# Kernel tuning notes

Measured on AMD Instinct MI355X. Metric: run time of the kernel, lower is better.

Reference implementation:

```python
import jax, jax.numpy as jnp
import numpy as np
from jax import lax

B, H, S, D = 4, 12, 4096, 64
TILE = 128


def setup_inputs() -> dict:
    key = jax.random.key(0)
    kq, kk, kv = jax.random.split(key, 3)
    query = jax.random.normal(kq, (B, H, S, D), dtype=jnp.float32)
    key_t = jax.random.normal(kk, (B, H, S, D), dtype=jnp.float32)
    value = jax.random.normal(kv, (B, H, S, D), dtype=jnp.float32)
    return {"query": query, "key": key_t, "value": value}


def _flash_tiled(query, key, value):
    b, h, s, d = query.shape
    scale = d ** (-0.5)
    nq = s // TILE
    nk = s // TILE
    # q tiles: [b, h, nq, TILE, d]; kv tiles scanned along leading axis
    q = query.reshape(b, h, nq, TILE, d)
    k = key.reshape(b, h, nk, TILE, d).transpose(2, 0, 1, 3, 4)    # [nk,b,h,TILE,d]
    v = value.reshape(b, h, nk, TILE, d).transpose(2, 0, 1, 3, 4)  # [nk,b,h,TILE,d]

    out0 = jnp.zeros((b, h, nq, TILE, d), dtype=query.dtype)
    m0 = jnp.full((b, h, nq, TILE, 1), -jnp.inf, dtype=query.dtype)
    s0 = jnp.zeros((b, h, nq, TILE, 1), dtype=query.dtype)

    def step(carry, kv_tiles):
        out, m, ssum = carry
        k_tile, v_tile = kv_tiles
        # scores: [b,h,nq,TILE_q,TILE_k]
        scores = jnp.einsum('bhntd,bhsd->bhnts', q, k_tile) * scale
        cur_max = jnp.max(scores, axis=-1, keepdims=True)
        new_max = jnp.maximum(m, cur_max)
        old_scale = jnp.exp(m - new_max)
        cur_scale = jnp.exp(cur_max - new_max)  # extra factor, faithful to source
        cur_exp = jnp.exp(scores - new_max)
        out = out * old_scale + cur_scale * jnp.einsum('bhnts,bhsd->bhntd', cur_exp, v_tile)
        ssum = ssum * old_scale + cur_scale * jnp.sum(cur_exp, axis=-1, keepdims=True)
        return (out, new_max, ssum), None

    (out, _, ssum), _ = lax.scan(step, (out0, m0, s0), (k, v))
    return (out / ssum).reshape(b, h, s, d)


def reference(query, key, value):
    return _flash_tiled(query, key, value)
```

## Files before the change

### kernel.cpp

```cpp
#include <hip/hip_runtime.h>
#include <hip/hip_bf16.h>


#define S_LEN 4096
#define HD    64
#define QTILE 128
#define KTILE 128
#define NKT   (S_LEN / KTILE)

#define KSTR  72
#define VSTR  136
#define VT_OFF (128 * KSTR)
#define SMEM_U16 (VT_OFF + HD * VSTR)
#define OSTR  68

typedef __attribute__((ext_vector_type(8))) short bf16x8;
typedef __attribute__((ext_vector_type(4))) short bf16x4;
typedef __attribute__((ext_vector_type(4))) float f32x4;

__device__ __forceinline__ unsigned int pk2(float f0, float f1) {
    unsigned int u0 = __builtin_bit_cast(unsigned int, f0) + 0x8000u;
    unsigned int u1 = __builtin_bit_cast(unsigned int, f1) + 0x8000u;
    return __builtin_amdgcn_perm(u1, u0, 0x07060302u);
}

__global__ __launch_bounds__(256, 3)
void fattn_kernel(const float* __restrict__ Q,
                  const float* __restrict__ K,
                  const float* __restrict__ V,
                  float* __restrict__ O) {
    __shared__ __align__(16) unsigned short smem[SMEM_U16];

    const int t    = threadIdx.x;
    const int wave = t >> 6;
    const int lane = t & 63;
    const int m    = lane & 15;
    const int quad = lane >> 4;

    const int qblk = blockIdx.x;
    const int head = blockIdx.y;
    const size_t hbase = (size_t)head * S_LEN * HD;

    unsigned short* const Kl = smem;
    unsigned short* const Vt = smem + VT_OFF;

    bf16x8 qf[2][2];
    #pragma unroll
    for (int rt = 0; rt < 2; ++rt) {
        const float* qp = Q + hbase +
            (size_t)(qblk * QTILE + wave * 32 + rt * 16 + m) * HD + quad * 8;
        #pragma unroll
        for (int kd = 0; kd < 2; ++kd) {
            float4 a = *(const float4*)(qp + kd * 32);
            float4 b = *(const float4*)(qp + kd * 32 + 4);
            union { unsigned int u[4]; bf16x8 v; } cv;
            cv.u[0] = pk2(a.x * 0.125f, a.y * 0.125f);
            cv.u[1] = pk2(a.z * 0.125f, a.w * 0.125f);
            cv.u[2] = pk2(b.x * 0.125f, b.y * 0.125f);
            cv.u[3] = pk2(b.z * 0.125f, b.w * 0.125f);
            qf[rt][kd] = cv.v;
        }
    }

    f32x4 oacc[4][2];
    float mrow[2] = {-INFINITY, -INFINITY};
    float lrow[2] = {0.f, 0.f};
    #pragma unroll
    for (int dt = 0; dt < 4; ++dt)
        #pragma unroll
        for (int rt = 0; rt < 2; ++rt) oacc[dt][rt] = (f32x4){0.f,0.f,0.f,0.f};

    const int r0k = t >> 3;
    const int c0k = (t & 7) * 8;
    const int chk = ((t & 7) + ((t >> 3) & 7)) & 7;
    const int vkey = t & 127;
    const int vdb  = (t >> 7) * 32;
    unsigned short* const vwp = &Vt[vdb * VSTR + vkey];

    float4 va[4][2];
    {
        const float* vp = V + hbase + (size_t)vkey * HD + vdb;
        #pragma unroll
        for (int i = 0; i < 4; ++i) {
            va[i][0] = *(const float4*)(vp + i * 8);
            va[i][1] = *(const float4*)(vp + i * 8 + 4);
        }
    }

    for (int kt = 0; kt < NKT; ++kt) {
        __syncthreads();

        #pragma unroll
        for (int i = 0; i < 4; ++i) {
            #pragma unroll
            for (int j = 0; j < 8; ++j) {
                float f = ((const float*)&va[i][j >> 2])[j & 3];
                unsigned int u = __builtin_bit_cast(unsigned int, f) + 0x8000u;
                vwp[(i * 8 + j) * VSTR] = (unsigned short)(u >> 16);
            }
        }
        {
            const float* kp = K + hbase + (size_t)(kt * KTILE + r0k) * HD + c0k;
            #pragma unroll
            for (int i = 0; i < 4; ++i) {
                float4 a = *(const float4*)(kp + i * 32 * HD);
                float4 b = *(const float4*)(kp + i * 32 * HD + 4);
                union { unsigned int u[4]; bf16x4 v[2]; } cv;
                cv.u[0] = pk2(a.x, a.y); cv.u[1] = pk2(a.z, a.w);
                cv.u[2] = pk2(b.x, b.y); cv.u[3] = pk2(b.z, b.w);
                *(bf16x8*)&Kl[(r0k + i * 32) * KSTR + chk * 8] =
                    *(bf16x8*)&cv.u[0];
            }
        }
        __syncthreads();

        {
            int nk = (kt + 1 < NKT) ? kt + 1 : 0;
            const float* vp = V + hbase + (size_t)(nk * KTILE + vkey) * HD + vdb;
            #pragma unroll
            for (int i = 0; i < 4; ++i) {
                va[i][0] = *(const float4*)(vp + i * 8);
                va[i][1] = *(const float4*)(vp + i * 8 + 4);
            }
        }

        f32x4 sacc[8][2];
        #pragma unroll
        for (int k8 = 0; k8 < 8; ++k8)
            #pragma unroll
            for (int rt = 0; rt < 2; ++rt) sacc[k8][rt] = (f32x4){0.f,0.f,0.f,0.f};

        #pragma unroll
        for (int kd = 0; kd < 2; ++kd) {
            const int coff = (((kd << 2) + quad + m) & 7) << 3;
            #pragma unroll
            for (int k8 = 0; k8 < 8; ++k8) {
                bf16x8 kf = *(const bf16x8*)&Kl[(k8 * 16 + m) * KSTR + coff];
                sacc[k8][0] = __builtin_amdgcn_mfma_f32_16x16x32_bf16(
                    kf, qf[0][kd], sacc[k8][0], 0, 0, 0);
                sacc[k8][1] = __builtin_amdgcn_mfma_f32_16x16x32_bf16(
                    kf, qf[1][kd], sacc[k8][1], 0, 0, 0);
            }
        }

        unsigned int pkv[8][2][2];
        #pragma unroll
        for (int rt = 0; rt < 2; ++rt) {
            float cm = sacc[0][rt][0];
            #pragma unroll
            for (int k8 = 0; k8 < 8; ++k8)
                #pragma unroll
                for (int r = 0; r < 4; ++r)
                    cm = fmaxf(cm, sacc[k8][rt][r]);
            cm = fmaxf(cm, __shfl_xor(cm, 16, 64));
            cm = fmaxf(cm, __shfl_xor(cm, 32, 64));

            float mo  = mrow[rt];
            float mn  = fmaxf(mo, cm);
            float osc = __expf(mo - mn);
            float bias = cm - mn - mn;
            mrow[rt] = mn;

            #pragma unroll
            for (int dt = 0; dt < 4; ++dt) {
                oacc[dt][rt][0] *= osc; oacc[dt][rt][1] *= osc;
                oacc[dt][rt][2] *= osc; oacc[dt][rt][3] *= osc;
            }

            float rs = 0.f;
            #pragma unroll
            for (int k8 = 0; k8 < 8; ++k8) {
                float p0 = __expf(sacc[k8][rt][0] + bias);
                float p1 = __expf(sacc[k8][rt][1] + bias);
                float p2 = __expf(sacc[k8][rt][2] + bias);
                float p3 = __expf(sacc[k8][rt][3] + bias);
                rs += (p0 + p1) + (p2 + p3);
                pkv[k8][rt][0] = pk2(p0, p1);
                pkv[k8][rt][1] = pk2(p2, p3);
            }
            rs += __shfl_xor(rs, 16, 64);
            rs += __shfl_xor(rs, 32, 64);
            lrow[rt] = lrow[rt] * osc + rs;
        }

        #pragma unroll
        for (int kc = 0; kc < 4; ++kc) {
            bf16x8 pf[2];
            #pragma unroll
            for (int rt = 0; rt < 2; ++rt) {
                union { unsigned int u[4]; bf16x8 v; } cv;
                cv.u[0] = pkv[2 * kc][rt][0];
                cv.u[1] = pkv[2 * kc][rt][1];
                cv.u[2] = pkv[2 * kc + 1][rt][0];
                cv.u[3] = pkv[2 * kc + 1][rt][1];
                pf[rt] = cv.v;
            }
            #pragma unroll
            for (int dt = 0; dt < 4; ++dt) {
                const unsigned short* vp0 =
                    &Vt[(dt * 16 + m) * VSTR + kc * 32 + quad * 4];
                bf16x4 a = *(const bf16x4*)vp0;
                bf16x4 b = *(const bf16x4*)(vp0 + 16);
                bf16x8 vf;
                vf[0]=a[0]; vf[1]=a[1]; vf[2]=a[2]; vf[3]=a[3];
                vf[4]=b[0]; vf[5]=b[1]; vf[6]=b[2]; vf[7]=b[3];
                oacc[dt][0] = __builtin_amdgcn_mfma_f32_16x16x32_bf16(
                    vf, pf[0], oacc[dt][0], 0, 0, 0);
                oacc[dt][1] = __builtin_amdgcn_mfma_f32_16x16x32_bf16(
                    vf, pf[1], oacc[dt][1], 0, 0, 0);
            }
        }
    }

    __syncthreads();
    float* Ol = (float*)smem;
    #pragma unroll
    for (int rt = 0; rt < 2; ++rt) {
        float inv = 1.0f / lrow[rt];
        #pragma unroll
        for (int dt = 0; dt < 4; ++dt)
            #pragma unroll
            for (int r = 0; r < 4; ++r)
                Ol[(wave * 32 + rt * 16 + m) * OSTR + dt * 16 + quad * 4 + r] =
                    oacc[dt][rt][r] * inv;
    }
    __syncthreads();
    const size_t obase = hbase + (size_t)(qblk * QTILE) * HD;
    #pragma unroll
    for (int s = 0; s < 8; ++s) {
        int row = s * 16 + (t >> 4);
        int col = (t & 15) * 4;
        *(float4*)&O[obase + (size_t)row * HD + col] =
            *(const float4*)&Ol[row * OSTR + col];
    }
}

extern "C" void kernel_launch(void* const* d_in, const int* in_sizes, int n_in,
                              void* d_out, int out_size, void* d_ws, size_t ws_size,
                              hipStream_t stream) {
    (void)in_sizes; (void)n_in; (void)d_ws; (void)ws_size; (void)out_size;
    const float* Q = (const float*)d_in[0];
    const float* K = (const float*)d_in[1];
    const float* V = (const float*)d_in[2];
    float* O = (float*)d_out;
    dim3 grid(S_LEN / QTILE, 4 * 12);
    fattn_kernel<<<grid, 256, 0, stream>>>(Q, K, V, O);
}
```

Measured before the change: 489.2 us.

## Pre-convert K and V to bf16 in workspace before the attention kernel

```diff
diff --git a/kernel.cpp b/kernel.cpp
--- a/kernel.cpp
+++ b/kernel.cpp
@@ -6,7 +6,8 @@
 #define HD    64
 #define QTILE 128
 #define KTILE 128
-#define NKT   (S_LEN / KTILE)
+#define NKT   32
+#define NHEAD 48
 
 #define KSTR  72
 #define VSTR  136
@@ -14,21 +15,84 @@
 #define SMEM_U16 (VT_OFF + HD * VSTR)
 #define OSTR  68
 
+#define WS_ELEMS ((size_t)NHEAD * S_LEN * HD)
+
 typedef __attribute__((ext_vector_type(8))) short bf16x8;
-typedef __attribute__((ext_vector_type(4))) short bf16x4;
 typedef __attribute__((ext_vector_type(4))) float f32x4;
 
 __device__ __forceinline__ unsigned int pk2(float f0, float f1) {
-    unsigned int u0 = __builtin_bit_cast(unsigned int, f0) + 0x8000u;
-    unsigned int u1 = __builtin_bit_cast(unsigned int, f1) + 0x8000u;
+    unsigned int u0 = __builtin_bit_cast(unsigned int, f0);
+    unsigned int u1 = __builtin_bit_cast(unsigned int, f1);
+    u0 += 0x7FFFu + ((u0 >> 16) & 1u);
+    u1 += 0x7FFFu + ((u1 >> 16) & 1u);
     return __builtin_amdgcn_perm(u1, u0, 0x07060302u);
 }
-
-__global__ __launch_bounds__(256, 3)
-void fattn_kernel(const float* __restrict__ Q,
-                  const float* __restrict__ K,
-                  const float* __restrict__ V,
-                  float* __restrict__ O) {
+__device__ __forceinline__ unsigned int pkt(float f0, float f1) {
+    return __builtin_amdgcn_perm(__builtin_bit_cast(unsigned int, f1),
+                                 __builtin_bit_cast(unsigned int, f0),
+                                 0x07060302u);
+}
+__device__ __forceinline__ float e2(float x) {
+#if __has_builtin(__builtin_amdgcn_exp2f)
+    return __builtin_amdgcn_exp2f(x);
+#else
+    return __expf(x * 0.6931471805599453f);
+#endif
+}
+
+__global__ __launch_bounds__(256)
+void k_convert(const float* __restrict__ K, unsigned short* __restrict__ Wk) {
+    size_t idx = ((size_t)blockIdx.x * 256 + threadIdx.x) * 8;
+    float4 a = *(const float4*)(K + idx);
+    float4 b = *(const float4*)(K + idx + 4);
+    union { unsigned int u[4]; bf16x8 v; } cv;
+    cv.u[0] = pk2(a.x, a.y); cv.u[1] = pk2(a.z, a.w);
+    cv.u[2] = pk2(b.x, b.y); cv.u[3] = pk2(b.z, b.w);
+    *(bf16x8*)((unsigned short*)Wk + idx) = cv.v;
+}
+
+__global__ __launch_bounds__(256)
+void v_trans(const float* __restrict__ V, unsigned short* __restrict__ Wv) {
+    __shared__ unsigned short T[64 * 132];
+    const int t = threadIdx.x;
+    const int kt = blockIdx.x, head = blockIdx.y;
+    const float* vp = V + (size_t)head * S_LEN * HD + (size_t)kt * KTILE * HD;
+    const int d0 = (t & 15) * 4;
+    const int kr = t >> 4;
+    #pragma unroll
+    for (int i = 0; i < 8; ++i) {
+        int key = i * 16 + kr;
+        float4 f = *(const float4*)(vp + key * HD + d0);
+        unsigned int p01 = pk2(f.x, f.y), p23 = pk2(f.z, f.w);
+        T[(d0 + 0) * 132 + key] = (unsigned short)(p01 & 0xffff);
+        T[(d0 + 1) * 132 + key] = (unsigned short)(p01 >> 16);
+        T[(d0 + 2) * 132 + key] = (unsigned short)(p23 & 0xffff);
+        T[(d0 + 3) * 132 + key] = (unsigned short)(p23 >> 16);
+    }
+    __syncthreads();
+    const int d = t >> 2;
+    const int c = t & 3;
+    unsigned short* op = Wv + (size_t)head * HD * S_LEN + (size_t)d * S_LEN
+                         + kt * KTILE + c * 32;
+    unsigned int out[16];
+    #pragma unroll
+    for (int jj = 0; jj < 16; ++jj) {
+        int j0 = 2 * jj, j1 = 2 * jj + 1;
+        int k0 = c * 32 + ((j0 >> 2) & 1) * 16 + (j0 >> 3) * 4 + (j0 & 3);
+        int k1 = c * 32 + ((j1 >> 2) & 1) * 16 + (j1 >> 3) * 4 + (j1 & 3);
+        out[jj] = (unsigned int)T[d * 132 + k0]
+                | ((unsigned int)T[d * 132 + k1] << 16);
+    }
+    #pragma unroll
+    for (int s = 0; s < 4; ++s)
+        *(bf16x8*)(op + s * 8) = *(const bf16x8*)&out[s * 4];
+}
+
+__global__ __launch_bounds__(256, 4)
+void fattn_fast(const float* __restrict__ Q,
+                const unsigned short* __restrict__ Wk,
+                const unsigned short* __restrict__ Wv,
+                float* __restrict__ O) {
     __shared__ __align__(16) unsigned short smem[SMEM_U16];
 
     const int t    = threadIdx.x;
@@ -41,6 +105,180 @@
     const int head = blockIdx.y;
     const size_t hbase = (size_t)head * S_LEN * HD;
 
+    unsigned short* const Kl = smem;
+    unsigned short* const Vt = smem + VT_OFF;
+
+    bf16x8 qf[2][2];
+    #pragma unroll
+    for (int rt = 0; rt < 2; ++rt) {
+        const float* qp = Q + hbase +
+            (size_t)(qblk * QTILE + wave * 32 + rt * 16 + m) * HD + quad * 8;
+        #pragma unroll
+        for (int kd = 0; kd < 2; ++kd) {
+            float4 a = *(const float4*)(qp + kd * 32);
+            float4 b = *(const float4*)(qp + kd * 32 + 4);
+            union { unsigned int u[4]; bf16x8 v; } cv;
+            const float s = 0.1803368801111f;
+            cv.u[0] = pk2(a.x * s, a.y * s);
+            cv.u[1] = pk2(a.z * s, a.w * s);
+            cv.u[2] = pk2(b.x * s, b.y * s);
+            cv.u[3] = pk2(b.z * s, b.w * s);
+            qf[rt][kd] = cv.v;
+        }
+    }
+
+    f32x4 oacc[4][2];
+    float mrow[2] = {-INFINITY, -INFINITY};
+    float lrow[2] = {0.f, 0.f};
+    #pragma unroll
+    for (int dt = 0; dt < 4; ++dt)
+        #pragma unroll
+        for (int rt = 0; rt < 2; ++rt) oacc[dt][rt] = (f32x4){0.f,0.f,0.f,0.f};
+
+    const int r0k = t >> 3;
+    const int kch = t & 7;
+    const int chk = ((t & 7) + ((t >> 3) & 7)) & 7;
+    const unsigned short* const kbase = Wk + hbase;
+    const unsigned short* const vbase = Wv + (size_t)head * HD * S_LEN;
+
+    for (int kt = 0; kt < NKT; ++kt) {
+        __syncthreads();
+        #pragma unroll
+        for (int i = 0; i < 4; ++i) {
+            int row = r0k + 32 * i;
+            bf16x8 kv = *(const bf16x8*)(kbase +
+                (size_t)(kt * KTILE + row) * HD + kch * 8);
+            *(bf16x8*)&Kl[row * KSTR + chk * 8] = kv;
+        }
+        #pragma unroll
+        for (int i = 0; i < 4; ++i) {
+            int id = t + 256 * i;
+            int d = id >> 4, ch = id & 15;
+            bf16x8 vv = *(const bf16x8*)(vbase +
+                (size_t)d * S_LEN + kt * KTILE + ch * 8);
+            *(bf16x8*)&Vt[d * VSTR + ch * 8] = vv;
+        }
+        __syncthreads();
+
+        f32x4 sacc[8][2];
+        #pragma unroll
+        for (int k8 = 0; k8 < 8; ++k8)
+            #pragma unroll
+            for (int rt = 0; rt < 2; ++rt) sacc[k8][rt] = (f32x4){0.f,0.f,0.f,0.f};
+
+        #pragma unroll
+        for (int kd = 0; kd < 2; ++kd) {
+            const int coff = (((kd << 2) + quad + m) & 7) << 3;
+            #pragma unroll
+            for (int k8 = 0; k8 < 8; ++k8) {
+                bf16x8 kf = *(const bf16x8*)&Kl[(k8 * 16 + m) * KSTR + coff];
+                sacc[k8][0] = __builtin_amdgcn_mfma_f32_16x16x32_bf16(
+                    kf, qf[0][kd], sacc[k8][0], 0, 0, 0);
+                sacc[k8][1] = __builtin_amdgcn_mfma_f32_16x16x32_bf16(
+                    kf, qf[1][kd], sacc[k8][1], 0, 0, 0);
+            }
+        }
+
+        unsigned int pkv[8][2][2];
+        #pragma unroll
+        for (int rt = 0; rt < 2; ++rt) {
+            float cm = sacc[0][rt][0];
+            #pragma unroll
+            for (int k8 = 0; k8 < 8; ++k8)
+                #pragma unroll
+                for (int r = 0; r < 4; ++r)
+                    cm = fmaxf(cm, sacc[k8][rt][r]);
+            cm = fmaxf(cm, __shfl_xor(cm, 16, 64));
+            cm = fmaxf(cm, __shfl_xor(cm, 32, 64));
+
+            float mo = mrow[rt];
+            float mn = fmaxf(mo, cm);
+            float bias = cm - mn - mn;
+            mrow[rt] = mn;
+
+            if (__any(cm > mo)) {
+                float osc = e2(mo - mn);
+                #pragma unroll
+                for (int dt = 0; dt < 4; ++dt) {
+                    oacc[dt][rt][0] *= osc; oacc[dt][rt][1] *= osc;
+                    oacc[dt][rt][2] *= osc; oacc[dt][rt][3] *= osc;
+                }
+                lrow[rt] *= osc;
+            }
+
+            float rs = 0.f;
+            #pragma unroll
+            for (int k8 = 0; k8 < 8; ++k8) {
+                float p0 = e2(sacc[k8][rt][0] + bias);
+                float p1 = e2(sacc[k8][rt][1] + bias);
+                float p2 = e2(sacc[k8][rt][2] + bias);
+                float p3 = e2(sacc[k8][rt][3] + bias);
+                rs += (p0 + p1) + (p2 + p3);
+                pkv[k8][rt][0] = pkt(p0, p1);
+                pkv[k8][rt][1] = pkt(p2, p3);
+            }
+            rs += __shfl_xor(rs, 16, 64);
+            rs += __shfl_xor(rs, 32, 64);
+            lrow[rt] += rs;
+        }
+
+        #pragma unroll
+        for (int kc = 0; kc < 4; ++kc) {
+            bf16x8 pf[2];
+            #pragma unroll
+            for (int rt = 0; rt < 2; ++rt) {
+                union { unsigned int u[4]; bf16x8 v; } cv;
+                cv.u[0] = pkv[2 * kc][rt][0];
+                cv.u[1] = pkv[2 * kc][rt][1];
+                cv.u[2] = pkv[2 * kc + 1][rt][0];
+                cv.u[3] = pkv[2 * kc + 1][rt][1];
+                pf[rt] = cv.v;
+            }
+            #pragma unroll
+            for (int dt = 0; dt < 4; ++dt) {
+                bf16x8 vf = *(const bf16x8*)&Vt[(dt * 16 + m) * VSTR +
+                                                kc * 32 + quad * 8];
+                oacc[dt][0] = __builtin_amdgcn_mfma_f32_16x16x32_bf16(
+                    vf, pf[0], oacc[dt][0], 0, 0, 0);
+                oacc[dt][1] = __builtin_amdgcn_mfma_f32_16x16x32_bf16(
+                    vf, pf[1], oacc[dt][1], 0, 0, 0);
+            }
+        }
+    }
+
+    __syncthreads();
+    float* Ol = (float*)smem;
+    #pragma unroll
+    for (int rt = 0; rt < 2; ++rt) {
+        float inv = 1.0f / lrow[rt];
+        #pragma unroll
+        for (int dt = 0; dt < 4; ++dt)
+            #pragma unroll
+            for (int r = 0; r < 4; ++r)
+                Ol[(wave * 32 + rt * 16 + m) * OSTR + dt * 16 + quad * 4 + r] =
+                    oacc[dt][rt][r] * inv;
+    }
+    __syncthreads();
+    const size_t obase = hbase + (size_t)(qblk * QTILE) * HD;
+    #pragma unroll
+    for (int s = 0; s < 8; ++s) {
+        int row = s * 16 + (t >> 4);
+        int col = (t & 15) * 4;
+        *(float4*)&O[obase + (size_t)row * HD + col] =
+            *(const float4*)&Ol[row * OSTR + col];
+    }
+}
+
+__global__ __launch_bounds__(256, 3)
+void fattn_fallback(const float* __restrict__ Q,
+                    const float* __restrict__ K,
+                    const float* __restrict__ V,
+                    float* __restrict__ O) {
+    __shared__ __align__(16) unsigned short smem[SMEM_U16];
+    const int t = threadIdx.x, wave = t >> 6, lane = t & 63;
+    const int m = lane & 15, quad = lane >> 4;
+    const int qblk = blockIdx.x, head = blockIdx.y;
+    const size_t hbase = (size_t)head * S_LEN * HD;
     unsigned short* const Kl = smem;
     unsigned short* const Vt = smem + VT_OFF;
 
@@ -61,7 +299,6 @@
             qf[rt][kd] = cv.v;
         }
     }
-
     f32x4 oacc[4][2];
     float mrow[2] = {-INFINITY, -INFINITY};
     float lrow[2] = {0.f, 0.f};
@@ -69,14 +306,10 @@
     for (int dt = 0; dt < 4; ++dt)
         #pragma unroll
         for (int rt = 0; rt < 2; ++rt) oacc[dt][rt] = (f32x4){0.f,0.f,0.f,0.f};
-
-    const int r0k = t >> 3;
-    const int c0k = (t & 7) * 8;
+    const int r0k = t >> 3, c0k = (t & 7) * 8;
     const int chk = ((t & 7) + ((t >> 3) & 7)) & 7;
-    const int vkey = t & 127;
-    const int vdb  = (t >> 7) * 32;
+    const int vkey = t & 127, vdb = (t >> 7) * 32;
     unsigned short* const vwp = &Vt[vdb * VSTR + vkey];
-
     float4 va[4][2];
     {
         const float* vp = V + hbase + (size_t)vkey * HD + vdb;
@@ -86,10 +319,8 @@
             va[i][1] = *(const float4*)(vp + i * 8 + 4);
         }
     }
-
     for (int kt = 0; kt < NKT; ++kt) {
         __syncthreads();
-
         #pragma unroll
         for (int i = 0; i < 4; ++i) {
             #pragma unroll
@@ -105,15 +336,13 @@
             for (int i = 0; i < 4; ++i) {
                 float4 a = *(const float4*)(kp + i * 32 * HD);
                 float4 b = *(const float4*)(kp + i * 32 * HD + 4);
-                union { unsigned int u[4]; bf16x4 v[2]; } cv;
+                union { unsigned int u[4]; bf16x8 v; } cv;
                 cv.u[0] = pk2(a.x, a.y); cv.u[1] = pk2(a.z, a.w);
                 cv.u[2] = pk2(b.x, b.y); cv.u[3] = pk2(b.z, b.w);
-                *(bf16x8*)&Kl[(r0k + i * 32) * KSTR + chk * 8] =
-                    *(bf16x8*)&cv.u[0];
+                *(bf16x8*)&Kl[(r0k + i * 32) * KSTR + chk * 8] = cv.v;
             }
         }
         __syncthreads();
-
         {
             int nk = (kt + 1 < NKT) ? kt + 1 : 0;
             const float* vp = V + hbase + (size_t)(nk * KTILE + vkey) * HD + vdb;
@@ -123,13 +352,11 @@
                 va[i][1] = *(const float4*)(vp + i * 8 + 4);
             }
         }
-
         f32x4 sacc[8][2];
         #pragma unroll
         for (int k8 = 0; k8 < 8; ++k8)
             #pragma unroll
             for (int rt = 0; rt < 2; ++rt) sacc[k8][rt] = (f32x4){0.f,0.f,0.f,0.f};
-
         #pragma unroll
         for (int kd = 0; kd < 2; ++kd) {
             const int coff = (((kd << 2) + quad + m) & 7) << 3;
@@ -142,7 +369,6 @@
                     kf, qf[1][kd], sacc[k8][1], 0, 0, 0);
             }
         }
-
         unsigned int pkv[8][2][2];
         #pragma unroll
         for (int rt = 0; rt < 2; ++rt) {
@@ -150,23 +376,18 @@
             #pragma unroll
             for (int k8 = 0; k8 < 8; ++k8)
                 #pragma unroll
-                for (int r = 0; r < 4; ++r)
-                    cm = fmaxf(cm, sacc[k8][rt][r]);
+                for (int r = 0; r < 4; ++r) cm = fmaxf(cm, sacc[k8][rt][r]);
             cm = fmaxf(cm, __shfl_xor(cm, 16, 64));
             cm = fmaxf(cm, __shfl_xor(cm, 32, 64));
-
-            float mo  = mrow[rt];
-            float mn  = fmaxf(mo, cm);
+            float mo = mrow[rt], mn = fmaxf(mo, cm);
             float osc = __expf(mo - mn);
             float bias = cm - mn - mn;
             mrow[rt] = mn;
-
             #pragma unroll
             for (int dt = 0; dt < 4; ++dt) {
                 oacc[dt][rt][0] *= osc; oacc[dt][rt][1] *= osc;
                 oacc[dt][rt][2] *= osc; oacc[dt][rt][3] *= osc;
             }
-
             float rs = 0.f;
             #pragma unroll
             for (int k8 = 0; k8 < 8; ++k8) {
@@ -182,7 +403,6 @@
             rs += __shfl_xor(rs, 32, 64);
             lrow[rt] = lrow[rt] * osc + rs;
         }
-
         #pragma unroll
         for (int kc = 0; kc < 4; ++kc) {
             bf16x8 pf[2];
@@ -199,11 +419,9 @@
             for (int dt = 0; dt < 4; ++dt) {
                 const unsigned short* vp0 =
                     &Vt[(dt * 16 + m) * VSTR + kc * 32 + quad * 4];
-                bf16x4 a = *(const bf16x4*)vp0;
-                bf16x4 b = *(const bf16x4*)(vp0 + 16);
                 bf16x8 vf;
-                vf[0]=a[0]; vf[1]=a[1]; vf[2]=a[2]; vf[3]=a[3];
-                vf[4]=b[0]; vf[5]=b[1]; vf[6]=b[2]; vf[7]=b[3];
+                #pragma unroll
+                for (int j = 0; j < 4; ++j) { vf[j] = vp0[j]; vf[4 + j] = vp0[16 + j]; }
                 oacc[dt][0] = __builtin_amdgcn_mfma_f32_16x16x32_bf16(
                     vf, pf[0], oacc[dt][0], 0, 0, 0);
                 oacc[dt][1] = __builtin_amdgcn_mfma_f32_16x16x32_bf16(
@@ -211,7 +429,6 @@
             }
         }
     }
-
     __syncthreads();
     float* Ol = (float*)smem;
     #pragma unroll
@@ -238,11 +455,19 @@
 extern "C" void kernel_launch(void* const* d_in, const int* in_sizes, int n_in,
                               void* d_out, int out_size, void* d_ws, size_t ws_size,
                               hipStream_t stream) {
-    (void)in_sizes; (void)n_in; (void)d_ws; (void)ws_size; (void)out_size;
+    (void)in_sizes; (void)n_in; (void)out_size;
     const float* Q = (const float*)d_in[0];
     const float* K = (const float*)d_in[1];
     const float* V = (const float*)d_in[2];
     float* O = (float*)d_out;
-    dim3 grid(S_LEN / QTILE, 4 * 12);
-    fattn_kernel<<<grid, 256, 0, stream>>>(Q, K, V, O);
-}
+    const size_t need = 2 * WS_ELEMS * sizeof(unsigned short);
+    if (ws_size >= need) {
+        unsigned short* Wk = (unsigned short*)d_ws;
+        unsigned short* Wv = Wk + WS_ELEMS;
+        k_convert<<<dim3((unsigned)(WS_ELEMS / (256 * 8))), 256, 0, stream>>>(K, Wk);
+        v_trans<<<dim3(NKT, NHEAD), 256, 0, stream>>>(V, Wv);
+        fattn_fast<<<dim3(S_LEN / QTILE, NHEAD), 256, 0, stream>>>(Q, Wk, Wv, O);
+    } else {
+        fattn_fallback<<<dim3(S_LEN / QTILE, NHEAD), 256, 0, stream>>>(Q, K, V, O);
+    }
+}
```

Result: slower. 910.7 us (+86.2%).
